# Performance work log

Measured on AMD Instinct MI355X. Metric: run time of the kernel, lower is better.

## Reference

```python
import jax, jax.numpy as jnp
import numpy as np

M, N, H, C = 32, 1024, 64, 10  # samples, nodes(==feature dim), hidden, classes
SLOPE = 0.2


def setup_inputs() -> dict:
    key = jax.random.key(0)
    ks = jax.random.split(key, 6)
    features = jax.random.normal(ks[0], (M, N, N), jnp.float32)           # [M, N, D], D == N
    weights = jax.random.uniform(ks[1], (M, N, N), jnp.float32)           # nonneg adjacency weights
    std = (2.0 / (1.0 + SLOPE ** 2) / N) ** 0.5                            # kaiming_normal for leaky_relu
    w_gnn0 = jax.random.normal(ks[2], (N, H), jnp.float32) * std
    w_gnn1 = jax.random.normal(ks[3], (N, H), jnp.float32) * std
    w_gnn2 = jax.random.normal(ks[4], (N, H), jnp.float32) * std
    fc_w = jax.random.normal(ks[5], (H, C), jnp.float32) * (1.0 / H ** 0.5)
    fc_b = jnp.zeros((C,), jnp.float32)
    return {
        "features": features,
        "weights": weights,
        "w_gnn0": w_gnn0,
        "w_gnn1": w_gnn1,
        "w_gnn2": w_gnn2,
        "fc_w": fc_w,
        "fc_b": fc_b,
        "view_flag": 0,
    }


def _forward(features, weights, w_gnn0, w_gnn1, w_gnn2, fc_w, fc_b, view_flag):
    Wg = (w_gnn0, w_gnn1, w_gnn2)[view_flag]  # static selection
    _, Nn, _ = features.shape
    Cc = fc_b.shape[0]
    eye = jnp.eye(Nn, dtype=features.dtype)
    rows = jnp.arange(Nn)

    def structural_enhancement(W, p):
        # Literal torch semantics: max_id is always 0 (scores_list[i] is 0-dim),
        # so rows i < p get column-0 entry set to 1 where > 0. Score/cos-sim
        # suppression never affects outputs (scores_list is discarded).
        col0 = W[:, 0]
        new_col0 = jnp.where((rows < p) & (col0 > 0), jnp.asarray(1.0, W.dtype), col0)
        return W.at[:, 0].set(new_col0)

    def per_sample(X, W0):
        XW = X @ Wg  # [N, H]; X and Wg are loop-invariant
        feat_s = jnp.zeros((Wg.shape[1],), X.dtype)
        sr_s = jnp.zeros((Cc,), X.dtype)
        b_s = jnp.zeros((Cc,), X.dtype)
        u_s = jnp.asarray(0.0, X.dtype)
        u0 = jnp.asarray(999.0, X.dtype)
        done = jnp.asarray(False)
        W = W0
        for t in range(1, 9):  # while-loop is bounded: break guaranteed at 5*t >= 40
            adjp = 0.5 * structural_enhancement(W, 5 * t) + eye  # [N, N]
            h = adjp @ XW                                         # [N, H]
            h = jnp.where(h >= 0, h, SLOPE * h)                   # leaky_relu (dropout p=0 / eval)
            feat = h.mean(axis=0)                                 # global avg pool over nodes -> [H]
            sr = jax.nn.softplus(feat @ fc_w + fc_b)              # [C]
            S = sr.sum() + Cc
            u = Cc / S
            brk = (u >= u0) | (5 * t >= 40)
            store = jnp.logical_and(~done, ~brk)
            W = jnp.where(store, adjp, W)
            u0 = jnp.where(store, u, u0)
            feat_s = jnp.where(store, feat, feat_s)
            sr_s = jnp.where(store, sr, sr_s)
            b_s = jnp.where(store, sr / S, b_s)
            u_s = jnp.where(store, u, u_s)
            done = jnp.logical_or(done, brk)
        return feat_s, W, sr_s, b_s, u_s

    return jax.vmap(per_sample)(features, weights)


def reference(features, weights, w_gnn0, w_gnn1, w_gnn2, fc_w, fc_b, view_flag):
    # returns (aft_feat [M,H], weights [M,N,N], single_results [M,C], bb [M,C], uu [M])
    return _forward(features, weights, w_gnn0, w_gnn1, w_gnn2, fc_w, fc_b, view_flag)
```

## Files before the change

kernel.cpp:

```cpp
#include <hip/hip_runtime.h>
#include <math.h>

#define MS 32
#define NN 1024
#define HH 64
#define CC 10
#define SLOPEF 0.2f

typedef __attribute__((ext_vector_type(8))) short bf16x8;
typedef __attribute__((ext_vector_type(4))) float f32x4;
typedef __attribute__((ext_vector_type(4))) unsigned int u32x4;

__device__ __forceinline__ void split2(float v, unsigned short& hi, unsigned short& lo) {
    unsigned u = __builtin_bit_cast(unsigned, v);
    hi = (unsigned short)(u >> 16);
    float hf = __builtin_bit_cast(float, u & 0xFFFF0000u);
    float l = v - hf;
    lo = (unsigned short)(__builtin_bit_cast(unsigned, l) >> 16);
}

__device__ __forceinline__ void transpose_split_img(
    const float* __restrict__ src,
    unsigned short* __restrict__ dh_img,
    unsigned short* __restrict__ dl_img)
{
    __shared__ float tile[64][65];
    const int t = threadIdx.x;
    #pragma unroll
    for (int q = 0; q < 4; ++q) {
        int lin = q * 256 + t;
        int r = lin >> 4;
        int c4 = (lin & 15) << 2;
        float4 v = *reinterpret_cast<const float4*>(src + (long)r * HH + c4);
        tile[r][c4 + 0] = v.x; tile[r][c4 + 1] = v.y;
        tile[r][c4 + 2] = v.z; tile[r][c4 + 3] = v.w;
    }
    __syncthreads();
    const int col = t >> 2;
    const int seg = t & 3;
    unsigned short h8[16], l8[16];
    #pragma unroll
    for (int j = 0; j < 16; ++j)
        split2(tile[seg * 16 + j][col], h8[j], l8[j]);
    int base = col * 128 + seg * 32;
    int swz  = (col & 7) << 4;
    *reinterpret_cast<u32x4*>((char*)dh_img + ((base +  0) ^ swz)) = *reinterpret_cast<u32x4*>(h8);
    *reinterpret_cast<u32x4*>((char*)dh_img + ((base + 16) ^ swz)) = *reinterpret_cast<u32x4*>(h8 + 8);
    *reinterpret_cast<u32x4*>((char*)dl_img + ((base +  0) ^ swz)) = *reinterpret_cast<u32x4*>(l8);
    *reinterpret_cast<u32x4*>((char*)dl_img + ((base + 16) ^ swz)) = *reinterpret_cast<u32x4*>(l8 + 8);
}

__global__ __launch_bounds__(256) void split_B_sel(
    const float* __restrict__ B0, const float* __restrict__ B1,
    const float* __restrict__ B2, const int* __restrict__ flag,
    unsigned short* __restrict__ dh, unsigned short* __restrict__ dl)
{
    int vf = flag[0];
    const float* B = (vf == 0) ? B0 : (vf == 1 ? B1 : B2);
    int c = blockIdx.x;
    transpose_split_img(B + (long)c * 64 * HH, dh + (long)c * 4096, dl + (long)c * 4096);
}

__global__ __launch_bounds__(256) void split_B_xw(
    const float* __restrict__ XWf,
    unsigned short* __restrict__ dh, unsigned short* __restrict__ dl)
{
    int m = blockIdx.y;
    int c = blockIdx.x;
    long so = (long)m * HH * NN;
    transpose_split_img(XWf + (long)m * NN * HH + (long)c * 64 * HH,
                        dh + so + (long)c * 4096, dl + so + (long)c * 4096);
}

template <int FUSED>
__global__ __launch_bounds__(256, 2) void gemm_split(
    const float* __restrict__ A, long aStride,
    const unsigned short* __restrict__ Bh, const unsigned short* __restrict__ Bl,
    long bStrideH,
    const float* __restrict__ XWf,
    float* __restrict__ Cmat)
{
    __shared__ __align__(16) unsigned short Ahi[4096];
    __shared__ __align__(16) unsigned short Alo[4096];
    __shared__ __align__(16) unsigned short Bhi[4096];
    __shared__ __align__(16) unsigned short Blo[4096];

    const int m = blockIdx.y;
    const int row0 = blockIdx.x * 64;
    const float* A_m = A + (long)m * aStride + (long)row0 * NN;
    const u32x4* bh4 = reinterpret_cast<const u32x4*>(Bh + (bStrideH ? (long)m * bStrideH : 0L));
    const u32x4* bl4 = reinterpret_cast<const u32x4*>(Bl + (bStrideH ? (long)m * bStrideH : 0L));

    const int tid = threadIdx.x;
    const int w   = tid >> 6;
    const int l   = tid & 63;
    const int l15 = l & 15;
    const int lg  = l >> 4;

    f32x4 acc[4] = {};

    int lin_r[4], lin_c4[4];
    #pragma unroll
    for (int q = 0; q < 4; ++q) {
        int lin = q * 256 + tid;
        lin_r[q]  = lin >> 4;
        lin_c4[q] = (lin & 15) << 2;
    }

    f32x4 av[4];
    u32x4 bhreg[2], blreg[2];
    #pragma unroll
    for (int q = 0; q < 4; ++q) {
        const f32x4* p = reinterpret_cast<const f32x4*>(A_m + (long)lin_r[q] * NN + lin_c4[q]);
        av[q] = FUSED ? *p : __builtin_nontemporal_load(p);
    }
    bhreg[0] = bh4[tid];       bhreg[1] = bh4[256 + tid];
    blreg[0] = bl4[tid];       blreg[1] = bl4[256 + tid];

    for (int kc = 0; kc < 16; ++kc) {
        #pragma unroll
        for (int q = 0; q < 4; ++q) {
            ushort4 h, lw;
            split2(av[q].x, h.x, lw.x);
            split2(av[q].y, h.y, lw.y);
            split2(av[q].z, h.z, lw.z);
            split2(av[q].w, h.w, lw.w);
            int byte = (lin_r[q] * 128 + lin_c4[q] * 2) ^ ((lin_r[q] & 7) << 4);
            *reinterpret_cast<ushort4*>((char*)Ahi + byte) = h;
            *reinterpret_cast<ushort4*>((char*)Alo + byte) = lw;
        }
        reinterpret_cast<u32x4*>(Bhi)[tid]       = bhreg[0];
        reinterpret_cast<u32x4*>(Bhi)[256 + tid] = bhreg[1];
        reinterpret_cast<u32x4*>(Blo)[tid]       = blreg[0];
        reinterpret_cast<u32x4*>(Blo)[256 + tid] = blreg[1];
        __syncthreads();

        if (kc < 15) {
            int ko = (kc + 1) * 64;
            #pragma unroll
            for (int q = 0; q < 4; ++q) {
                const f32x4* p = reinterpret_cast<const f32x4*>(A_m + (long)lin_r[q] * NN + ko + lin_c4[q]);
                av[q] = FUSED ? *p : __builtin_nontemporal_load(p);
            }
            int cb = (kc + 1) * 512;
            bhreg[0] = bh4[cb + tid];       bhreg[1] = bh4[cb + 256 + tid];
            blreg[0] = bl4[cb + tid];       blreg[1] = bl4[cb + 256 + tid];
        }

        #pragma unroll
        for (int s = 0; s < 2; ++s) {
            int arow  = w * 16 + l15;
            int abyte = (arow * 128 + s * 64 + lg * 16) ^ ((arow & 7) << 4);
            bf16x8 ah = *reinterpret_cast<bf16x8*>((char*)Ahi + abyte);
            bf16x8 al = *reinterpret_cast<bf16x8*>((char*)Alo + abyte);
            #pragma unroll
            for (int fc = 0; fc < 4; ++fc) {
                int col   = fc * 16 + l15;
                int bbyte = (col * 128 + s * 64 + lg * 16) ^ ((col & 7) << 4);
                bf16x8 bh8 = *reinterpret_cast<bf16x8*>((char*)Bhi + bbyte);
                bf16x8 bl8 = *reinterpret_cast<bf16x8*>((char*)Blo + bbyte);
                acc[fc] = __builtin_amdgcn_mfma_f32_16x16x32_bf16(ah, bh8, acc[fc], 0, 0, 0);
                acc[fc] = __builtin_amdgcn_mfma_f32_16x16x32_bf16(ah, bl8, acc[fc], 0, 0, 0);
                acc[fc] = __builtin_amdgcn_mfma_f32_16x16x32_bf16(al, bh8, acc[fc], 0, 0, 0);
            }
        }
        __syncthreads();
    }

    if constexpr (!FUSED) {
        float* C_m = Cmat + (long)m * NN * HH + (long)row0 * HH;
        #pragma unroll
        for (int fc = 0; fc < 4; ++fc) {
            #pragma unroll
            for (int r = 0; r < 4; ++r) {
                int row = w * 16 + lg * 4 + r;
                int col = fc * 16 + l15;
                C_m[(long)row * HH + col] = acc[fc][r];
            }
        }
    } else {
        __shared__ float x0s[64];
        __shared__ float red2[4][8][64];
        const float* XWm = XWf + (long)m * NN * HH;
        if (tid < 64) x0s[tid] = XWm[tid];
        __syncthreads();

        int grows[4]; float v[4], bc[4];
        #pragma unroll
        for (int r = 0; r < 4; ++r) {
            int lrow = w * 16 + lg * 4 + r;
            grows[r] = row0 + lrow;
            v[r] = A[(long)m * aStride + (long)grows[r] * NN];
            bc[r] = 0.0f;
        }
        float xwv[4][4];
        #pragma unroll
        for (int fc = 0; fc < 4; ++fc) {
            int col = fc * 16 + l15;
            #pragma unroll
            for (int r = 0; r < 4; ++r)
                xwv[fc][r] = XWm[(long)grows[r] * HH + col];
        }

        float alpha = 1.0f, gamma = 0.0f;
        #pragma unroll
        for (int t = 1; t <= 8; ++t) {
            #pragma unroll
            for (int r = 0; r < 4; ++r) {
                float c = (grows[r] < 5 * t && v[r] > 0.0f) ? (1.0f - v[r]) : 0.0f;
                bc[r] = 0.5f * (bc[r] + c);
                v[r]  = 0.5f * (v[r] + c) + (grows[r] == 0 ? 1.0f : 0.0f);
            }
            alpha *= 0.5f;
            gamma = 0.5f * gamma + 1.0f;
            #pragma unroll
            for (int fc = 0; fc < 4; ++fc) {
                float x0c = x0s[fc * 16 + l15];
                float s = 0.0f;
                #pragma unroll
                for (int r = 0; r < 4; ++r) {
                    float y = alpha * acc[fc][r] + bc[r] * x0c + gamma * xwv[fc][r];
                    s += (y >= 0.0f) ? y : SLOPEF * y;
                }
                s += __shfl_xor(s, 16);
                s += __shfl_xor(s, 32);
                if (l < 16) red2[w][t - 1][fc * 16 + l] = s;
            }
        }
        __syncthreads();
        if (tid < 512) {
            int t8 = tid >> 6, col = tid & 63;
            float p = red2[0][t8][col] + red2[1][t8][col] +
                      red2[2][t8][col] + red2[3][t8][col];
            Cmat[(((long)m * 16 + blockIdx.x) * 8 + t8) * 64 + col] = p;
        }
    }
}

__global__ __launch_bounds__(512) void decide_kernel(
    const float* __restrict__ partials,
    const float* __restrict__ weights,
    const float* __restrict__ fc_w,
    const float* __restrict__ fc_b,
    float* __restrict__ col0k,
    int* __restrict__ k_arr,
    float* __restrict__ out_feat,
    float* __restrict__ out_sr,
    float* __restrict__ out_b,
    float* __restrict__ out_u)
{
    __shared__ float feat[8][64];
    __shared__ float sr_all[8][CC];
    __shared__ float Ss[8], us[8];
    __shared__ int ksh;

    const int m = blockIdx.x;
    const int tid = threadIdx.x;

    {
        int t8 = tid >> 6, col = tid & 63;
        float s = 0.0f;
        for (int bx = 0; bx < 16; ++bx)
            s += partials[(((long)m * 16 + bx) * 8 + t8) * 64 + col];
        feat[t8][col] = s * (1.0f / NN);
    }
    __syncthreads();

    if (tid < 80) {
        int t8 = tid / 10, c = tid % 10;
        float a = fc_b[c];
        for (int h = 0; h < HH; ++h) a += feat[t8][h] * fc_w[h * CC + c];
        sr_all[t8][c] = log1pf(expf(-fabsf(a))) + fmaxf(a, 0.0f);
    }
    __syncthreads();

    if (tid < 8) {
        float S = (float)CC;
        for (int c = 0; c < CC; ++c) S += sr_all[tid][c];
        Ss[tid] = S;
        us[tid] = (float)CC / S;
    }
    __syncthreads();

    if (tid == 0) {
        float u0 = 999.0f; int k = 1;
        for (int tt = 1; tt <= 8; ++tt) {
            float u = us[tt - 1];
            int brk = (u >= u0) || (tt == 8);
            if (!brk) { k = tt; u0 = u; } else break;
        }
        ksh = k;
        k_arr[m] = k;
        out_u[m] = us[k - 1];
    }
    __syncthreads();

    const int k = ksh;
    if (tid < 64) out_feat[m * HH + tid] = feat[k - 1][tid];
    if (tid < CC) {
        out_sr[m * CC + tid] = sr_all[k - 1][tid];
        out_b[m * CC + tid]  = sr_all[k - 1][tid] / Ss[k - 1];
    }
    for (int i = tid; i < NN; i += 512) {
        float v = weights[(long)m * NN * NN + (long)i * NN];
        for (int s = 1; s <= k; ++s) {
            float c = (i < 5 * s && v > 0.0f) ? (1.0f - v) : 0.0f;
            v = 0.5f * (v + c) + (i == 0 ? 1.0f : 0.0f);
        }
        col0k[m * NN + i] = v;
    }
}

__global__ __launch_bounds__(256) void finalize_W(
    const float* __restrict__ W0, const float* __restrict__ col0k,
    const int* __restrict__ k_arr, float* __restrict__ outW)
{
    const long n4 = (long)MS * NN * NN / 4;
    const long stride = (long)gridDim.x * 256;
    for (long i4 = (long)blockIdx.x * 256 + threadIdx.x; i4 < n4; i4 += stride) {
        long e = i4 * 4;
        int m = (int)(e >> 20);
        int i = (int)((e >> 10) & 1023);
        int j = (int)(e & 1023);
        int k = k_arr[m];
        float scale = 1.0f / (float)(1 << k);
        float diagadd = 2.0f * (1.0f - scale);

        f32x4 wv = reinterpret_cast<const f32x4*>(W0)[i4];
        float v0 = scale * wv.x + ((i == j + 0) ? diagadd : 0.0f);
        float v1 = scale * wv.y + ((i == j + 1) ? diagadd : 0.0f);
        float v2 = scale * wv.z + ((i == j + 2) ? diagadd : 0.0f);
        float v3 = scale * wv.w + ((i == j + 3) ? diagadd : 0.0f);
        if (j == 0) v0 = col0k[m * NN + i];
        f32x4 o = {v0, v1, v2, v3};
        __builtin_nontemporal_store(o, reinterpret_cast<f32x4*>(outW) + i4);
    }
}

extern "C" void kernel_launch(void* const* d_in, const int* in_sizes, int n_in,
                              void* d_out, int out_size, void* d_ws, size_t ws_size,
                              hipStream_t stream)
{
    const float* features = (const float*)d_in[0];
    const float* weights  = (const float*)d_in[1];
    const float* w_gnn0   = (const float*)d_in[2];
    const float* w_gnn1   = (const float*)d_in[3];
    const float* w_gnn2   = (const float*)d_in[4];
    const float* fc_w     = (const float*)d_in[5];
    const float* fc_b     = (const float*)d_in[6];
    const int*   viewFlag = (const int*)d_in[7];

    float* out = (float*)d_out;
    float* out_feat = out;
    float* outW     = out + (long)MS * HH;
    float* out_sr   = outW + (long)MS * NN * NN;
    float* out_b    = out_sr + MS * CC;
    float* out_u    = out_b + MS * CC;

    float* wsf = (float*)d_ws;
    float* XWf            = wsf;
    unsigned short* XWh   = (unsigned short*)(XWf + (long)MS * NN * HH);
    unsigned short* XWl   = XWh + (long)MS * HH * NN;
    unsigned short* Wgh   = XWl + (long)MS * HH * NN;
    unsigned short* Wgl   = Wgh + (long)HH * NN;
    float* partials       = (float*)(Wgl + (long)HH * NN);
    float* col0k          = partials + (long)MS * 16 * 8 * 64;
    int*   k_arr          = (int*)(col0k + (long)MS * NN);

    split_B_sel<<<16, 256, 0, stream>>>(w_gnn0, w_gnn1, w_gnn2, viewFlag, Wgh, Wgl);
    dim3 gemmGrid(NN / 64, MS);
    gemm_split<0><<<gemmGrid, 256, 0, stream>>>(features, (long)NN * NN,
                                                Wgh, Wgl, 0L, nullptr, XWf);
    split_B_xw<<<dim3(16, MS), 256, 0, stream>>>(XWf, XWh, XWl);
    gemm_split<1><<<gemmGrid, 256, 0, stream>>>(weights, (long)NN * NN,
                                                XWh, XWl, (long)HH * NN, XWf, partials);
    decide_kernel<<<MS, 512, 0, stream>>>(partials, weights, fc_w, fc_b,
                                          col0k, k_arr,
                                          out_feat, out_sr, out_b, out_u);
    finalize_W<<<2048, 256, 0, stream>>>(weights, col0k, k_arr, outW);
}
```

Baseline: 124.4 us.

## Fuse XW hi/lo split into first GEMM epilogue and share LDS buffers

The first GEMM's epilogue now splits its fp32 accumulators into bf16 hi/lo parts and writes them directly in the transposed, swizzled layout. This removes the separate split_B_xw kernel launch and its re-read of XW. Shared memory is consolidated into one 32KB buffer that the fused epilogue reuses for its reduction scratch. Launch bounds are raised to 4 blocks per CU to improve occupancy, which may cost registers and cause spills.

Result: no change. 122.0 us (-1.9%).

```diff
diff --git a/kernel.cpp b/kernel.cpp
--- a/kernel.cpp
+++ b/kernel.cpp
@@ -19,11 +19,18 @@
     lo = (unsigned short)(__builtin_bit_cast(unsigned, l) >> 16);
 }
 
-__device__ __forceinline__ void transpose_split_img(
-    const float* __restrict__ src,
-    unsigned short* __restrict__ dh_img,
-    unsigned short* __restrict__ dl_img)
-{
+__global__ __launch_bounds__(256) void split_B_sel(
+    const float* __restrict__ B0, const float* __restrict__ B1,
+    const float* __restrict__ B2, const int* __restrict__ flag,
+    unsigned short* __restrict__ dh, unsigned short* __restrict__ dl)
+{
+    int vf = flag[0];
+    const float* B = (vf == 0) ? B0 : (vf == 1 ? B1 : B2);
+    int c = blockIdx.x;
+    const float* src = B + (long)c * 64 * HH;
+    unsigned short* dh_img = dh + (long)c * 4096;
+    unsigned short* dl_img = dl + (long)c * 4096;
+
     __shared__ float tile[64][65];
     const int t = threadIdx.x;
     #pragma unroll
@@ -50,40 +57,21 @@
     *reinterpret_cast<u32x4*>((char*)dl_img + ((base + 16) ^ swz)) = *reinterpret_cast<u32x4*>(l8 + 8);
 }
 
-__global__ __launch_bounds__(256) void split_B_sel(
-    const float* __restrict__ B0, const float* __restrict__ B1,
-    const float* __restrict__ B2, const int* __restrict__ flag,
-    unsigned short* __restrict__ dh, unsigned short* __restrict__ dl)
-{
-    int vf = flag[0];
-    const float* B = (vf == 0) ? B0 : (vf == 1 ? B1 : B2);
-    int c = blockIdx.x;
-    transpose_split_img(B + (long)c * 64 * HH, dh + (long)c * 4096, dl + (long)c * 4096);
-}
-
-__global__ __launch_bounds__(256) void split_B_xw(
-    const float* __restrict__ XWf,
-    unsigned short* __restrict__ dh, unsigned short* __restrict__ dl)
-{
-    int m = blockIdx.y;
-    int c = blockIdx.x;
-    long so = (long)m * HH * NN;
-    transpose_split_img(XWf + (long)m * NN * HH + (long)c * 64 * HH,
-                        dh + so + (long)c * 4096, dl + so + (long)c * 4096);
-}
-
-template <int FUSED>
-__global__ __launch_bounds__(256, 2) void gemm_split(
+template <int MODE>
+__global__ __launch_bounds__(256, 4) void gemm_split(
     const float* __restrict__ A, long aStride,
     const unsigned short* __restrict__ Bh, const unsigned short* __restrict__ Bl,
     long bStrideH,
     const float* __restrict__ XWf,
+    unsigned short* __restrict__ ChOut,
+    unsigned short* __restrict__ ClOut,
     float* __restrict__ Cmat)
 {
-    __shared__ __align__(16) unsigned short Ahi[4096];
-    __shared__ __align__(16) unsigned short Alo[4096];
-    __shared__ __align__(16) unsigned short Bhi[4096];
-    __shared__ __align__(16) unsigned short Blo[4096];
+    __shared__ __align__(16) char smem[32768];
+    unsigned short* Ahi = (unsigned short*)(smem);
+    unsigned short* Alo = (unsigned short*)(smem + 8192);
+    unsigned short* Bhi = (unsigned short*)(smem + 16384);
+    unsigned short* Blo = (unsigned short*)(smem + 24576);
 
     const int m = blockIdx.y;
     const int row0 = blockIdx.x * 64;
@@ -112,7 +100,7 @@
     #pragma unroll
     for (int q = 0; q < 4; ++q) {
         const f32x4* p = reinterpret_cast<const f32x4*>(A_m + (long)lin_r[q] * NN + lin_c4[q]);
-        av[q] = FUSED ? *p : __builtin_nontemporal_load(p);
+        av[q] = (MODE == 1) ? *p : __builtin_nontemporal_load(p);
     }
     bhreg[0] = bh4[tid];       bhreg[1] = bh4[256 + tid];
     blreg[0] = bl4[tid];       blreg[1] = bl4[256 + tid];
@@ -140,7 +128,7 @@
             #pragma unroll
             for (int q = 0; q < 4; ++q) {
                 const f32x4* p = reinterpret_cast<const f32x4*>(A_m + (long)lin_r[q] * NN + ko + lin_c4[q]);
-                av[q] = FUSED ? *p : __builtin_nontemporal_load(p);
+                av[q] = (MODE == 1) ? *p : __builtin_nontemporal_load(p);
             }
             int cb = (kc + 1) * 512;
             bhreg[0] = bh4[cb + tid];       bhreg[1] = bh4[cb + 256 + tid];
@@ -167,20 +155,31 @@
         __syncthreads();
     }
 
-    if constexpr (!FUSED) {
+    if constexpr (MODE == 0) {
         float* C_m = Cmat + (long)m * NN * HH + (long)row0 * HH;
+        unsigned short* dh = ChOut + (long)m * HH * NN + (long)blockIdx.x * 4096;
+        unsigned short* dl = ClOut + (long)m * HH * NN + (long)blockIdx.x * 4096;
+        const int kb = (w * 16 + lg * 4) * 2;
         #pragma unroll
         for (int fc = 0; fc < 4; ++fc) {
+            int col = fc * 16 + l15;
+            ushort4 h4, l4;
+            split2(acc[fc][0], h4.x, l4.x);
+            split2(acc[fc][1], h4.y, l4.y);
+            split2(acc[fc][2], h4.z, l4.z);
+            split2(acc[fc][3], h4.w, l4.w);
             #pragma unroll
             for (int r = 0; r < 4; ++r) {
                 int row = w * 16 + lg * 4 + r;
-                int col = fc * 16 + l15;
                 C_m[(long)row * HH + col] = acc[fc][r];
             }
+            int byte = (col * 128 + kb) ^ ((col & 7) << 4);
+            *reinterpret_cast<ushort4*>((char*)dh + byte) = h4;
+            *reinterpret_cast<ushort4*>((char*)dl + byte) = l4;
         }
     } else {
-        __shared__ float x0s[64];
-        __shared__ float red2[4][8][64];
+        float* red2 = (float*)(smem);
+        float* x0s  = (float*)(smem + 8192);
         const float* XWm = XWf + (long)m * NN * HH;
         if (tid < 64) x0s[tid] = XWm[tid];
         __syncthreads();
@@ -224,14 +223,14 @@
                 }
                 s += __shfl_xor(s, 16);
                 s += __shfl_xor(s, 32);
-                if (l < 16) red2[w][t - 1][fc * 16 + l] = s;
+                if (l < 16) red2[(w * 8 + (t - 1)) * 64 + fc * 16 + l] = s;
             }
         }
         __syncthreads();
         if (tid < 512) {
             int t8 = tid >> 6, col = tid & 63;
-            float p = red2[0][t8][col] + red2[1][t8][col] +
-                      red2[2][t8][col] + red2[3][t8][col];
+            float p = red2[(0 * 8 + t8) * 64 + col] + red2[(1 * 8 + t8) * 64 + col] +
+                      red2[(2 * 8 + t8) * 64 + col] + red2[(3 * 8 + t8) * 64 + col];
             Cmat[(((long)m * 16 + blockIdx.x) * 8 + t8) * 64 + col] = p;
         }
     }
@@ -370,10 +369,11 @@
     split_B_sel<<<16, 256, 0, stream>>>(w_gnn0, w_gnn1, w_gnn2, viewFlag, Wgh, Wgl);
     dim3 gemmGrid(NN / 64, MS);
     gemm_split<0><<<gemmGrid, 256, 0, stream>>>(features, (long)NN * NN,
-                                                Wgh, Wgl, 0L, nullptr, XWf);
-    split_B_xw<<<dim3(16, MS), 256, 0, stream>>>(XWf, XWh, XWl);
+                                                Wgh, Wgl, 0L, nullptr,
+                                                XWh, XWl, XWf);
     gemm_split<1><<<gemmGrid, 256, 0, stream>>>(weights, (long)NN * NN,
-                                                XWh, XWl, (long)HH * NN, XWf, partials);
+                                                XWh, XWl, (long)HH * NN, XWf,
+                                                nullptr, nullptr, partials);
     decide_kernel<<<MS, 512, 0, stream>>>(partials, weights, fc_w, fc_b,
                                           col0k, k_arr,
                                           out_feat, out_sr, out_b, out_u);
```
